# Kernel tuning notes

Measured on AMD Instinct MI355X. Metric: run time of the kernel, lower is better.

Reference implementation:

```python
import jax, jax.numpy as jnp
import numpy as np
from jax import lax

IMG_SIZE = 512        # efficientdet-d0 input resolution
TOP_K = 256           # fixed candidate count for jit-compatible NMS
THRESHOLD = 0.01      # score threshold (init kwarg)
IOU_THRESHOLD = 0.5   # NMS IoU threshold (init kwarg)


def make_anchors():
    """Standard EfficientDet-d0 anchors: P3-P7, 3 scales x 3 ratios, xyxy."""
    strides = [8, 16, 32, 64, 128]
    scales = [2.0 ** 0, 2.0 ** (1.0 / 3.0), 2.0 ** (2.0 / 3.0)]
    ratios = [0.5, 1.0, 2.0]
    base = 4.0
    out = []
    for s in strides:
        fs = IMG_SIZE // s
        xs = (np.arange(fs, dtype=np.float32) + 0.5) * s
        cy, cx = np.meshgrid(xs, xs, indexing='ij')
        for r in ratios:
            for sc in scales:
                w = base * s * sc * np.sqrt(1.0 / r)
                h = base * s * sc * np.sqrt(r)
                a = np.stack([cx - w / 2, cy - h / 2, cx + w / 2, cy + h / 2], -1)
                out.append(a.reshape(-1, 4))
    return np.concatenate(out, 0).astype(np.float32)  # [49104, 4]


def decode_boxes(anchors, regs):
    """RetinaNet-style delta decode. anchors [A,4] xyxy, regs [B,A,4]."""
    aw = anchors[:, 2] - anchors[:, 0]
    ah = anchors[:, 3] - anchors[:, 1]
    acx = anchors[:, 0] + 0.5 * aw
    acy = anchors[:, 1] + 0.5 * ah
    dx, dy, dw, dh = regs[..., 0], regs[..., 1], regs[..., 2], regs[..., 3]
    cx = acx + dx * aw
    cy = acy + dy * ah
    w = aw * jnp.exp(jnp.clip(dw, -4.0, 4.0))
    h = ah * jnp.exp(jnp.clip(dh, -4.0, 4.0))
    boxes = jnp.stack([cx - 0.5 * w, cy - 0.5 * h, cx + 0.5 * w, cy + 0.5 * h], -1)
    return jnp.clip(boxes, 0.0, float(IMG_SIZE))  # [B,A,4]


def pairwise_iou(boxes):
    """boxes [K,4] xyxy -> iou [K,K]."""
    area = jnp.maximum(boxes[:, 2] - boxes[:, 0], 0) * jnp.maximum(boxes[:, 3] - boxes[:, 1], 0)
    lt = jnp.maximum(boxes[:, None, :2], boxes[None, :, :2])
    rb = jnp.minimum(boxes[:, None, 2:], boxes[None, :, 2:])
    wh = jnp.maximum(rb - lt, 0.0)
    inter = wh[..., 0] * wh[..., 1]
    union = area[:, None] + area[None, :] - inter
    return inter / jnp.maximum(union, 1e-8)


def nms_keep(boxes, scores):
    """Sequential NMS over score-sorted candidates. boxes [K,4], scores [K]."""
    K = boxes.shape[0]
    iou = pairwise_iou(boxes)  # [K,K]
    ar = jnp.arange(K)
    keep0 = scores > 0.0

    def body(i, keep):
        suppressed = jnp.any(keep & (iou[:, i] > IOU_THRESHOLD) & (ar < i))
        return keep.at[i].set(keep[i] & ~suppressed)

    return lax.fori_loop(0, K, body, keep0)


def setup_inputs() -> dict:
    key = jax.random.key(0)
    k1, k2 = jax.random.split(key)
    B, A, C = 8, 49104, 80
    cls_logits = jax.random.normal(k1, (B, A, C), dtype=jnp.float32) - 2.0
    box_regs = 0.2 * jax.random.normal(k2, (B, A, 4), dtype=jnp.float32)
    anchors = jnp.asarray(make_anchors())
    return {"cls_logits": cls_logits, "box_regs": box_regs, "anchors": anchors}


def reference(cls_logits, box_regs, anchors):
    probs = jax.nn.sigmoid(cls_logits)            # [B,A,C]
    scores = probs.max(-1)                        # [B,A]
    labels = probs.argmax(-1)                     # [B,A]
    boxes = decode_boxes(anchors, box_regs)       # [B,A,4]
    scores = jnp.where(scores > THRESHOLD, scores, 0.0)
    top_s, idx = lax.top_k(scores, TOP_K)         # [B,K]
    top_b = jnp.take_along_axis(boxes, idx[..., None], axis=1)   # [B,K,4]
    top_l = jnp.take_along_axis(labels, idx, axis=1)             # [B,K]
    keep = jax.vmap(nms_keep)(top_b, top_s)                      # [B,K] bool
    keep_f = keep.astype(top_b.dtype)
    dets = jnp.concatenate([top_b * keep_f[..., None], (top_s * keep_f)[..., None]], -1)  # [B,K,5]
    return dets, top_l, keep
```

## Files before the change

### kernel.cpp

```cpp
#include <hip/hip_runtime.h>
#include <stdint.h>
#include <math.h>

#define IMGF   512.0f
#define A_N    49104
#define B_N    8
#define C_N    80
#define K_N    256
#define IOU_T  0.5f
#define NBIN   16384
#define CAP    2048
#define NPAIR  (B_N * A_N / 2)

__device__ __forceinline__ int bin_of(uint32_t key) {
    float s = __uint_as_float(key);
    int b = (int)(s * 16384.0f);
    return b > 16383 ? 16383 : b;
}

__global__ __launch_bounds__(256) void score_kernel(
    const float* __restrict__ logits,
    uint32_t* __restrict__ keys,
    int* __restrict__ labels)
{
    const int tid  = threadIdx.x;
    const int lane = tid & 63;
    const int grp  = lane >> 2, j = lane & 3;
    const int ggid = blockIdx.x * 64 + (tid >> 6) * 16 + grp;
    const int NGt  = gridDim.x * 64;

    float4 c[10];
    int p = ggid;
    {
        const float4* r = (const float4*)(logits + (size_t)(2 * p) * C_N);
#pragma unroll
        for (int k = 0; k < 5; ++k) { c[k] = r[j + 4 * k]; c[5 + k] = r[20 + j + 4 * k]; }
    }
    while (true) {
        const int pn = p + NGt;
        const bool vn = pn < NPAIR;
        float4 n[10];
        if (vn) {
            const float4* r = (const float4*)(logits + (size_t)(2 * pn) * C_N);
#pragma unroll
            for (int k = 0; k < 5; ++k) { n[k] = r[j + 4 * k]; n[5 + k] = r[20 + j + 4 * k]; }
        }
        {
            const float* f = (const float*)c;
            float m0 = f[0], m1 = f[20];
#pragma unroll
            for (int q = 1; q < 20; ++q) m0 = fmaxf(m0, f[q]);
#pragma unroll
            for (int q = 1; q < 20; ++q) m1 = fmaxf(m1, f[20 + q]);
            m0 = fmaxf(m0, __shfl_xor(m0, 1, 64));
            m0 = fmaxf(m0, __shfl_xor(m0, 2, 64));
            m1 = fmaxf(m1, __shfl_xor(m1, 1, 64));
            m1 = fmaxf(m1, __shfl_xor(m1, 2, 64));
            int cl0 = 1 << 30, cl1 = 1 << 30;
#pragma unroll
            for (int k = 0; k < 5; ++k) {
#pragma unroll
                for (int q = 0; q < 4; ++q) {
                    const int cc = (j + 4 * k) * 4 + q;
                    const float v0 = ((const float*)&c[k])[q];
                    const float v1 = ((const float*)&c[5 + k])[q];
                    if (v0 == m0 && cc < cl0) cl0 = cc;
                    if (v1 == m1 && cc < cl1) cl1 = cc;
                }
            }
            { int t = __shfl_xor(cl0, 1, 64); if (t < cl0) cl0 = t;
              t = __shfl_xor(cl0, 2, 64); if (t < cl0) cl0 = t; }
            { int t = __shfl_xor(cl1, 1, 64); if (t < cl1) cl1 = t;
              t = __shfl_xor(cl1, 2, 64); if (t < cl1) cl1 = t; }
            if (j < 2) {
                const float m = (j == 0) ? m0 : m1;
                const int  cl = (j == 0) ? cl0 : cl1;
                float s = 1.0f / (1.0f + expf(-m));
                if (!(s > 0.01f)) s = 0.0f;
                const int row = 2 * p + j;
                keys[row]   = __float_as_uint(s);
                labels[row] = cl;
            }
        }
        if (!vn) break;
#pragma unroll
        for (int q = 0; q < 10; ++q) c[q] = n[q];
        p = pn;
    }
}

__global__ __launch_bounds__(1024) void select_nms_kernel(
    const uint32_t* __restrict__ keys,
    const int* __restrict__ labels,
    const float* __restrict__ regs,
    const float* __restrict__ anchors,
    float* __restrict__ out)
{
    const int b   = blockIdx.x;
    const int tid = threadIdx.x;

    __shared__ uint32_t hist[NBIN];
    __shared__ int ssum[1024];
    __shared__ int sh_T, sh_nc;
    __shared__ unsigned long long cand[CAP];
    __shared__ unsigned long long sorted[K_N];
    __shared__ float4 sbox[K_N];
    __shared__ float  sscore[K_N];
    __shared__ int    slab[K_N];
    __shared__ unsigned long long supr[K_N][4];
    __shared__ unsigned long long keepw[4];

    const uint32_t* kb = keys + (size_t)b * A_N;
    const uint4* kb4 = (const uint4*)kb;
    const int N4 = A_N / 4;

    for (int i = tid; i < NBIN; i += 1024) hist[i] = 0;
    __syncthreads();
    for (int i = tid; i < N4; i += 1024) {
        uint4 v = kb4[i];
        atomicAdd(&hist[bin_of(v.x)], 1u);
        atomicAdd(&hist[bin_of(v.y)], 1u);
        atomicAdd(&hist[bin_of(v.z)], 1u);
        atomicAdd(&hist[bin_of(v.w)], 1u);
    }
    __syncthreads();

    const int lo = tid * (NBIN / 1024);
    int seg = 0;
#pragma unroll
    for (int q = 0; q < NBIN / 1024; ++q) seg += (int)hist[lo + q];
    ssum[tid] = seg;
    __syncthreads();
    for (int off = 1; off < 1024; off <<= 1) {
        int v = (tid + off < 1024) ? ssum[tid + off] : 0;
        __syncthreads();
        ssum[tid] += v;
        __syncthreads();
    }
    int above = ssum[tid] - seg;
    if (above < K_N && above + seg >= K_N) {
        int cum = above;
        for (int bin = lo + NBIN / 1024 - 1; bin >= lo; --bin) {
            int c = (int)hist[bin];
            if (cum + c >= K_N) { sh_T = bin; break; }
            cum += c;
        }
    }
    if (tid == 0) sh_nc = 0;
    __syncthreads();
    const int T = sh_T;

    for (int i = tid; i < N4; i += 1024) {
        uint4 v = kb4[i];
        uint32_t ks[4] = { v.x, v.y, v.z, v.w };
#pragma unroll
        for (int q = 0; q < 4; ++q) {
            if (bin_of(ks[q]) >= T) {
                int p = atomicAdd(&sh_nc, 1);
                if (p < CAP)
                    cand[p] = ((unsigned long long)ks[q] << 32)
                            | (unsigned long long)(0xFFFFFFFFu - (uint32_t)(4 * i + q));
            }
        }
    }
    if (tid < K_N) sorted[tid] = 0ull;
    __syncthreads();
    int nc = sh_nc; if (nc > CAP) nc = CAP;

    for (int i = tid; i < nc; i += 1024) {
        unsigned long long me = cand[i];
        int r = 0;
        for (int jq = 0; jq < nc; ++jq) r += (cand[jq] > me);
        if (r < K_N) sorted[r] = me;
    }
    __syncthreads();

    if (tid < K_N) {
#pragma clang fp contract(off)
        unsigned long long cv = sorted[tid];
        uint32_t key = (uint32_t)(cv >> 32);
        uint32_t ai  = 0xFFFFFFFFu - (uint32_t)cv;
        if (ai >= (uint32_t)A_N) ai = 0;
        int a = (int)ai;
        float s = __uint_as_float(key);
        sscore[tid] = s;
        slab[tid]   = labels[(size_t)b * A_N + a];

        float ax0 = anchors[4 * a + 0], ay0 = anchors[4 * a + 1];
        float ax1 = anchors[4 * a + 2], ay1 = anchors[4 * a + 3];
        float aw = ax1 - ax0, ah = ay1 - ay0;
        float acx = ax0 + 0.5f * aw, acy = ay0 + 0.5f * ah;
        const float* r = regs + ((size_t)b * A_N + a) * 4;
        float dx = r[0], dy = r[1], dw = r[2], dh = r[3];
        float cx = acx + dx * aw;
        float cy = acy + dy * ah;
        dw = fminf(fmaxf(dw, -4.0f), 4.0f);
        dh = fminf(fmaxf(dh, -4.0f), 4.0f);
        float w = aw * expf(dw);
        float h = ah * expf(dh);
        float x0 = cx - 0.5f * w, y0 = cy - 0.5f * h;
        float x1 = cx + 0.5f * w, y1 = cy + 0.5f * h;
        x0 = fminf(fmaxf(x0, 0.0f), IMGF);
        y0 = fminf(fmaxf(y0, 0.0f), IMGF);
        x1 = fminf(fmaxf(x1, 0.0f), IMGF);
        y1 = fminf(fmaxf(y1, 0.0f), IMGF);
        sbox[tid] = make_float4(x0, y0, x1, y1);
    }
    __syncthreads();

    {
#pragma clang fp contract(off)
        const int row = tid & 255, gq = tid >> 8;
        float4 bi = sbox[row];
        float areai = fmaxf(bi.z - bi.x, 0.0f) * fmaxf(bi.w - bi.y, 0.0f);
        unsigned long long m = 0;
        const int jlo = gq * 64, jhi = jlo + 64;
        int start = row + 1 > jlo ? row + 1 : jlo;
        for (int jx = start; jx < jhi; ++jx) {
            float4 bj = sbox[jx];
            float areaj = fmaxf(bj.z - bj.x, 0.0f) * fmaxf(bj.w - bj.y, 0.0f);
            float lx = fmaxf(bi.x, bj.x), ly = fmaxf(bi.y, bj.y);
            float rx = fminf(bi.z, bj.z), ry = fminf(bi.w, bj.w);
            float iw = fmaxf(rx - lx, 0.0f), ih = fmaxf(ry - ly, 0.0f);
            float inter = iw * ih;
            float uni = areai + areaj - inter;
            float iou = inter / fmaxf(uni, 1e-8f);
            if (iou > IOU_T) m |= 1ull << (jx & 63);
        }
        supr[row][gq] = m;
    }
    if (tid < K_N) {
        unsigned long long ball = __ballot(sscore[tid] > 0.0f);
        if ((tid & 63) == 0) keepw[tid >> 6] = ball;
    }
    __syncthreads();

    if (tid == 0) {
        unsigned long long k0 = keepw[0], k1 = keepw[1], k2 = keepw[2], k3 = keepw[3];
#define NMS_CHUNK(c, kc)                                                     \
        for (int l = 0; l < 64; ++l) {                                       \
            const int i = (c) * 64 + l;                                      \
            unsigned long long w0 = supr[i][0], w1 = supr[i][1];             \
            unsigned long long w2 = supr[i][2], w3 = supr[i][3];             \
            if ((kc >> l) & 1ull) {                                          \
                k0 &= ~w0; k1 &= ~w1; k2 &= ~w2; k3 &= ~w3;                  \
            }                                                                \
        }
        NMS_CHUNK(0, k0)
        NMS_CHUNK(1, k1)
        NMS_CHUNK(2, k2)
        NMS_CHUNK(3, k3)
#undef NMS_CHUNK
        keepw[0] = k0; keepw[1] = k1; keepw[2] = k2; keepw[3] = k3;
    }
    __syncthreads();

    if (tid < K_N) {
        float keepf = ((keepw[tid >> 6] >> (tid & 63)) & 1ull) ? 1.0f : 0.0f;
        float4 bx = sbox[tid];
        float s = sscore[tid];
        float* det = out + ((size_t)b * K_N + tid) * 5;
        det[0] = bx.x * keepf;
        det[1] = bx.y * keepf;
        det[2] = bx.z * keepf;
        det[3] = bx.w * keepf;
        det[4] = s * keepf;
        out[(size_t)B_N * K_N * 5 + (size_t)b * K_N + tid] = (float)slab[tid];
        out[(size_t)B_N * K_N * 5 + (size_t)B_N * K_N + (size_t)b * K_N + tid] = keepf;
    }
}

extern "C" void kernel_launch(void* const* d_in, const int* in_sizes, int n_in,
                              void* d_out, int out_size, void* d_ws, size_t ws_size,
                              hipStream_t stream)
{
    const float* logits  = (const float*)d_in[0];
    const float* regs    = (const float*)d_in[1];
    const float* anchors = (const float*)d_in[2];
    float* out = (float*)d_out;

    uint32_t* keys   = (uint32_t*)d_ws;
    int*      labels = (int*)(keys + (size_t)B_N * A_N);

    score_kernel<<<768, 256, 0, stream>>>(logits, keys, labels);
    select_nms_kernel<<<B_N, 1024, 0, stream>>>(keys, labels, regs, anchors, out);
}
```

Before: 239.7 us.

## Defer argmax to top-K candidates and simplify score kernel and histogram scan

The score kernel now computes only the per-anchor max and score, with one quad of lanes per anchor and one launch per row group instead of a pipelined grid-stride loop. Labels are no longer written for every anchor; the argmax is recomputed only for the 256 selected candidates by rereading their logits in the select kernel. The histogram shrinks from 16384 to 4096 bins, and the block-wide shared-memory suffix scan is replaced by wave shuffles plus per-wave totals. The coarser bins can put more candidates above the threshold, which raises the risk of exceeding the candidate cap and makes the O(n^2) rank sort more expensive.

```diff
diff --git a/kernel.cpp b/kernel.cpp
--- a/kernel.cpp
+++ b/kernel.cpp
@@ -8,99 +8,53 @@
 #define C_N    80
 #define K_N    256
 #define IOU_T  0.5f
-#define NBIN   16384
+#define NBIN   4096
 #define CAP    2048
-#define NPAIR  (B_N * A_N / 2)
 
 __device__ __forceinline__ int bin_of(uint32_t key) {
     float s = __uint_as_float(key);
-    int b = (int)(s * 16384.0f);
-    return b > 16383 ? 16383 : b;
+    int b = (int)(s * 4096.0f);
+    return b > 4095 ? 4095 : b;
 }
 
 __global__ __launch_bounds__(256) void score_kernel(
     const float* __restrict__ logits,
-    uint32_t* __restrict__ keys,
-    int* __restrict__ labels)
+    uint32_t* __restrict__ keys)
 {
     const int tid  = threadIdx.x;
     const int lane = tid & 63;
     const int grp  = lane >> 2, j = lane & 3;
-    const int ggid = blockIdx.x * 64 + (tid >> 6) * 16 + grp;
-    const int NGt  = gridDim.x * 64;
-
-    float4 c[10];
-    int p = ggid;
-    {
-        const float4* r = (const float4*)(logits + (size_t)(2 * p) * C_N);
-#pragma unroll
-        for (int k = 0; k < 5; ++k) { c[k] = r[j + 4 * k]; c[5 + k] = r[20 + j + 4 * k]; }
-    }
-    while (true) {
-        const int pn = p + NGt;
-        const bool vn = pn < NPAIR;
-        float4 n[10];
-        if (vn) {
-            const float4* r = (const float4*)(logits + (size_t)(2 * pn) * C_N);
-#pragma unroll
-            for (int k = 0; k < 5; ++k) { n[k] = r[j + 4 * k]; n[5 + k] = r[20 + j + 4 * k]; }
-        }
-        {
-            const float* f = (const float*)c;
-            float m0 = f[0], m1 = f[20];
-#pragma unroll
-            for (int q = 1; q < 20; ++q) m0 = fmaxf(m0, f[q]);
-#pragma unroll
-            for (int q = 1; q < 20; ++q) m1 = fmaxf(m1, f[20 + q]);
-            m0 = fmaxf(m0, __shfl_xor(m0, 1, 64));
-            m0 = fmaxf(m0, __shfl_xor(m0, 2, 64));
-            m1 = fmaxf(m1, __shfl_xor(m1, 1, 64));
-            m1 = fmaxf(m1, __shfl_xor(m1, 2, 64));
-            int cl0 = 1 << 30, cl1 = 1 << 30;
-#pragma unroll
-            for (int k = 0; k < 5; ++k) {
-#pragma unroll
-                for (int q = 0; q < 4; ++q) {
-                    const int cc = (j + 4 * k) * 4 + q;
-                    const float v0 = ((const float*)&c[k])[q];
-                    const float v1 = ((const float*)&c[5 + k])[q];
-                    if (v0 == m0 && cc < cl0) cl0 = cc;
-                    if (v1 == m1 && cc < cl1) cl1 = cc;
-                }
-            }
-            { int t = __shfl_xor(cl0, 1, 64); if (t < cl0) cl0 = t;
-              t = __shfl_xor(cl0, 2, 64); if (t < cl0) cl0 = t; }
-            { int t = __shfl_xor(cl1, 1, 64); if (t < cl1) cl1 = t;
-              t = __shfl_xor(cl1, 2, 64); if (t < cl1) cl1 = t; }
-            if (j < 2) {
-                const float m = (j == 0) ? m0 : m1;
-                const int  cl = (j == 0) ? cl0 : cl1;
-                float s = 1.0f / (1.0f + expf(-m));
-                if (!(s > 0.01f)) s = 0.0f;
-                const int row = 2 * p + j;
-                keys[row]   = __float_as_uint(s);
-                labels[row] = cl;
-            }
-        }
-        if (!vn) break;
-#pragma unroll
-        for (int q = 0; q < 10; ++q) c[q] = n[q];
-        p = pn;
+    const int g = blockIdx.x * 64 + (tid >> 6) * 16 + grp;
+
+    const float4* p = (const float4*)(logits + (size_t)g * C_N);
+    float4 v0 = p[j], v1 = p[j + 4], v2 = p[j + 8], v3 = p[j + 12], v4 = p[j + 16];
+    float m = fmaxf(fmaxf(fmaxf(v0.x, v0.y), fmaxf(v0.z, v0.w)),
+                    fmaxf(fmaxf(v1.x, v1.y), fmaxf(v1.z, v1.w)));
+    m = fmaxf(m, fmaxf(fmaxf(v2.x, v2.y), fmaxf(v2.z, v2.w)));
+    m = fmaxf(m, fmaxf(fmaxf(v3.x, v3.y), fmaxf(v3.z, v3.w)));
+    m = fmaxf(m, fmaxf(fmaxf(v4.x, v4.y), fmaxf(v4.z, v4.w)));
+    m = fmaxf(m, __shfl_xor(m, 1, 64));
+    m = fmaxf(m, __shfl_xor(m, 2, 64));
+    if (j == 0) {
+        float s = 1.0f / (1.0f + expf(-m));
+        if (!(s > 0.01f)) s = 0.0f;
+        keys[g] = __float_as_uint(s);
     }
 }
 
 __global__ __launch_bounds__(1024) void select_nms_kernel(
     const uint32_t* __restrict__ keys,
-    const int* __restrict__ labels,
+    const float* __restrict__ logits,
     const float* __restrict__ regs,
     const float* __restrict__ anchors,
     float* __restrict__ out)
 {
     const int b   = blockIdx.x;
     const int tid = threadIdx.x;
+    const int lane = tid & 63, wv = tid >> 6;
 
     __shared__ uint32_t hist[NBIN];
-    __shared__ int ssum[1024];
+    __shared__ int wtots[16];
     __shared__ int sh_T, sh_nc;
     __shared__ unsigned long long cand[CAP];
     __shared__ unsigned long long sorted[K_N];
@@ -115,6 +69,7 @@
     const int N4 = A_N / 4;
 
     for (int i = tid; i < NBIN; i += 1024) hist[i] = 0;
+    if (tid == 0) sh_nc = 0;
     __syncthreads();
     for (int i = tid; i < N4; i += 1024) {
         uint4 v = kb4[i];
@@ -125,28 +80,28 @@
     }
     __syncthreads();
 
-    const int lo = tid * (NBIN / 1024);
-    int seg = 0;
+    const int lo = tid * 4;
+    int seg = (int)hist[lo] + (int)hist[lo + 1]
+            + (int)hist[lo + 2] + (int)hist[lo + 3];
+    int s1 = seg;
 #pragma unroll
-    for (int q = 0; q < NBIN / 1024; ++q) seg += (int)hist[lo + q];
-    ssum[tid] = seg;
-    __syncthreads();
-    for (int off = 1; off < 1024; off <<= 1) {
-        int v = (tid + off < 1024) ? ssum[tid + off] : 0;
-        __syncthreads();
-        ssum[tid] += v;
-        __syncthreads();
-    }
-    int above = ssum[tid] - seg;
+    for (int off = 1; off < 64; off <<= 1) {
+        int v = __shfl_down(s1, off, 64);
+        if (lane + off < 64) s1 += v;
+    }
+    if (lane == 0) wtots[wv] = s1;
+    __syncthreads();
+    int wsuf = 0;
+    for (int w = wv + 1; w < 16; ++w) wsuf += wtots[w];
+    int above = wsuf + (s1 - seg);
     if (above < K_N && above + seg >= K_N) {
         int cum = above;
-        for (int bin = lo + NBIN / 1024 - 1; bin >= lo; --bin) {
+        for (int bin = lo + 3; bin >= lo; --bin) {
             int c = (int)hist[bin];
             if (cum + c >= K_N) { sh_T = bin; break; }
             cum += c;
         }
     }
-    if (tid == 0) sh_nc = 0;
     __syncthreads();
     const int T = sh_T;
 
@@ -184,7 +139,20 @@
         int a = (int)ai;
         float s = __uint_as_float(key);
         sscore[tid] = s;
-        slab[tid]   = labels[(size_t)b * A_N + a];
+
+        {
+            const float4* lp = (const float4*)(logits + ((size_t)b * A_N + a) * C_N);
+            float best = -INFINITY; int cls = 0;
+#pragma unroll
+            for (int k = 0; k < 20; ++k) {
+                float4 w = lp[k];
+                if (w.x > best) { best = w.x; cls = 4 * k + 0; }
+                if (w.y > best) { best = w.y; cls = 4 * k + 1; }
+                if (w.z > best) { best = w.z; cls = 4 * k + 2; }
+                if (w.w > best) { best = w.w; cls = 4 * k + 3; }
+            }
+            slab[tid] = cls;
+        }
 
         float ax0 = anchors[4 * a + 0], ay0 = anchors[4 * a + 1];
         float ax1 = anchors[4 * a + 2], ay1 = anchors[4 * a + 3];
@@ -279,9 +247,9 @@
     const float* anchors = (const float*)d_in[2];
     float* out = (float*)d_out;
 
-    uint32_t* keys   = (uint32_t*)d_ws;
-    int*      labels = (int*)(keys + (size_t)B_N * A_N);
-
-    score_kernel<<<768, 256, 0, stream>>>(logits, keys, labels);
-    select_nms_kernel<<<B_N, 1024, 0, stream>>>(keys, labels, regs, anchors, out);
-}
+    uint32_t* keys = (uint32_t*)d_ws;
+
+    const int total = B_N * A_N;
+    score_kernel<<<total / 64, 256, 0, stream>>>(logits, keys);
+    select_nms_kernel<<<B_N, 1024, 0, stream>>>(keys, logits, regs, anchors, out);
+}
```

Result: no change. 237.8 us (-0.8%).
